# Optimization experiments

Hardware: AMD Instinct MI355X
Metric: run time of the kernel (lower is better)

The kernel has to match this reference:

```python
import jax, jax.numpy as jnp
import numpy as np

K = 16  # topK from config


def setup_inputs() -> dict:
    key = jax.random.key(0)
    k1, k2 = jax.random.split(key)
    predictions = jax.random.uniform(k1, (8, 256, 8), dtype=jnp.float32)
    ref_imgs = jax.random.uniform(k2, (8, 3, 192, 192), dtype=jnp.float32)
    return {"predictions": predictions, "ref_imgs": ref_imgs}


def _dist_loss(predictions, ref_imgs):
    bs, L, _ = predictions.shape
    ch, H, W = ref_imgs.shape[1], ref_imgs.shape[2], ref_imgs.shape[3]
    img_size = W  # original uses ref_imgs.shape[-1] for both axes
    pos = predictions[:, :, :2]  # (bs, L, 2), normalized (x, y) in [0, 1]

    # --- nearest grid_sample (align_corners=False, padding zeros) ---
    # Faithful to the original einops mixup: flat sample i uses image i % bs
    # and grid point preds.reshape(bs*L, 2)[i].
    grid = pos.reshape(bs * L, 2)
    img_idx = jnp.arange(bs * L) % bs
    # unnormalize: pix = ((2g - 1) + 1) * S / 2 - 0.5 = g * S - 0.5
    ix = jnp.round(grid[:, 0] * W - 0.5).astype(jnp.int32)
    iy = jnp.round(grid[:, 1] * H - 0.5).astype(jnp.int32)
    inb = ((ix >= 0) & (ix < W) & (iy >= 0) & (iy < H)).astype(ref_imgs.dtype)
    ixc = jnp.clip(ix, 0, W - 1)
    iyc = jnp.clip(iy, 0, H - 1)
    pooled_flat = ref_imgs[img_idx, :, iyc, ixc] * inb[:, None]  # (bs*L, ch)
    # pooled_colors rearranged '(L bs) ch 1 1 -> bs L ch' with flat order (L outer, bs inner)
    pooled = pooled_flat.reshape(L, bs, ch).transpose(1, 0, 2)  # (bs, L, ch)

    # --- per-pixel squared color distance, sum over channels ---
    # ||ref - pooled||^2 = ||ref||^2 - 2<ref, pooled> + ||pooled||^2 (avoids (bs,L,ch,H,W))
    ref_sq = jnp.sum(ref_imgs * ref_imgs, axis=1)  # (bs, H, W)
    cross = jnp.einsum('bchw,blc->blhw', ref_imgs, pooled)  # (bs, L, H, W)
    pooled_sq = jnp.sum(pooled * pooled, axis=-1)  # (bs, L)
    similar = ref_sq[:, None] - 2.0 * cross + pooled_sq[:, :, None, None]

    # --- K most-similar pixel locations ---
    _, idx = jax.lax.top_k(-similar.reshape(bs, L, H * W), K)  # smallest K
    tgt_x = (idx % img_size).astype(pos.dtype) / img_size
    tgt_y = (idx // img_size).astype(pos.dtype) / img_size
    tgt = jnp.stack([tgt_x, tgt_y], axis=-1)  # (bs, L, K, 2)
    tgt_down = jnp.roll(tgt, shift=1, axis=1)

    # --- closest candidate of the previous stroke (positions detached) ---
    pd = jax.lax.stop_gradient(pos)[:, :, None, :]  # (bs, L, 1, 2)
    dist_down = jnp.sum((pd - tgt_down) ** 2, axis=-1)  # (bs, L, K)
    closest = jnp.argmin(dist_down, axis=-1)  # (bs, L)
    final_tgt = jnp.take_along_axis(tgt_down, closest[:, :, None, None], axis=2)[:, :, 0, :]

    loss = jnp.sum((pos[:, 1:] - final_tgt[:, 1:]) ** 2, axis=-1)  # (bs, L-1)
    return jnp.mean(loss)


def reference(predictions, ref_imgs):
    return _dist_loss(predictions, ref_imgs)
```

## Files before the change

### kernel.cpp

```cpp
#include <hip/hip_runtime.h>
#include <stdint.h>

#define BS 8
#define HH 192
#define WW 192
#define HW (HH*WW)
#define KK 16
#define SITES 9216
#define NW 16
#define SEGSZ 64
#define UCAP 512
#define PAD_FILT 4e-5f

typedef unsigned long long u64;


__device__ __forceinline__ uint32_t fkey(float f) {
    uint32_t u = __float_as_uint(f);
    uint32_t mask = (uint32_t)((int32_t)u >> 31) | 0x80000000u;
    return u ^ mask;
}
__device__ __forceinline__ float inv_fkey(uint32_t v) {
    uint32_t u = (v & 0x80000000u) ? (v ^ 0x80000000u) : ~v;
    return __uint_as_float(u);
}

__device__ __forceinline__ u64 umin64(u64 a, u64 b) { return a < b ? a : b; }

__device__ __forceinline__ uint32_t mbcnt64(u64 m) {
    return __builtin_amdgcn_mbcnt_hi((uint32_t)(m >> 32),
            __builtin_amdgcn_mbcnt_lo((uint32_t)m, 0));
}

__device__ __forceinline__ u64 wave_min_u64(u64 v) {
    #pragma unroll
    for (int off = 32; off >= 1; off >>= 1) {
        uint32_t lo = (uint32_t)v, hi = (uint32_t)(v >> 32);
        lo = __shfl_xor(lo, off, 64);
        hi = __shfl_xor(hi, off, 64);
        u64 o = ((u64)hi << 32) | lo;
        v = umin64(v, o);
    }
    return v;
}

__device__ __forceinline__ void insert64(u64 (&kept)[KK], u64 key) {
    #pragma unroll
    for (int j = KK - 1; j >= 1; --j) {
        u64 a = kept[j - 1];
        u64 mn = umin64(kept[j], key);
        kept[j] = (key < a) ? a : mn;
    }
    kept[0] = umin64(kept[0], key);
}

__device__ __forceinline__ float exact_rsq(float a, float b, float c) {
    return __fadd_rn(__fadd_rn(__fmul_rn(a, a), __fmul_rn(b, b)), __fmul_rn(c, c));
}
__device__ __forceinline__ float exact_sim(float c0, float c1, float c2, float rsq, float4 pq) {
    float cr = __fadd_rn(__fadd_rn(__fmul_rn(c0, pq.x), __fmul_rn(c1, pq.y)), __fmul_rn(c2, pq.z));
    return __fadd_rn(__fsub_rn(rsq, __fmul_rn(2.0f, cr)), pq.w);
}

#define LOSS_STEP(gmv)                                                   \
{                                                                        \
    uint32_t idxv = (uint32_t)(gmv);                                     \
    float tx = (float)(idxv % WW) / 192.0f;                              \
    float ty = (float)(idxv / WW) / 192.0f;                              \
    float ddx = __fsub_rn(px1, tx);                                      \
    float ddy = __fsub_rn(py1, ty);                                      \
    float dd = __fadd_rn(__fmul_rn(ddx, ddx), __fmul_rn(ddy, ddy));      \
    if (dd < dmin) { dmin = dd; btx = tx; bty = ty; }                    \
}

__global__ __launch_bounds__(1024) void fused_kernel(const float* __restrict__ pred,
                                                     const float* __restrict__ ref,
                                                     float* __restrict__ partial) {
    __shared__ uint32_t seg[8 * NW * SEGSZ];
    __shared__ uint32_t compactb[8 * UCAP];
    __shared__ uint32_t scnts[8 * NW];
    __shared__ float4 spool[8];
    __shared__ float sh[8];

    int tid  = threadIdx.x;
    int lane = tid & 63;
    int wid  = tid >> 6;
    int b  = blockIdx.x & 7;
    int qg = blockIdx.x >> 3;

    if (tid < 8) {
        int l = qg * 8 + tid;
        int i = l * BS + b;
        int b2 = i >> 8, l2 = i & 255;
        const float* pr = pred + ((b2 * 256 + l2) * 8);
        float x = pr[0], y = pr[1];
        float fx = rintf(__fsub_rn(__fmul_rn(x, 192.0f), 0.5f));
        float fy = rintf(__fsub_rn(__fmul_rn(y, 192.0f), 0.5f));
        int ix = (int)fx, iy = (int)fy;
        int inb = (ix >= 0 && ix < WW && iy >= 0 && iy < HH) ? 1 : 0;
        int ixc = min(max(ix, 0), WW - 1);
        int iyc = min(max(iy, 0), HH - 1);
        float m = (float)inb;
        const float* img = ref + b * 3 * HW + iyc * WW + ixc;
        float p0 = __fmul_rn(img[0], m);
        float p1 = __fmul_rn(img[HW], m);
        float p2 = __fmul_rn(img[2 * HW], m);
        float psq = __fadd_rn(__fadd_rn(__fmul_rn(p0, p0), __fmul_rn(p1, p1)),
                              __fmul_rn(p2, p2));
        spool[tid] = make_float4(p0, p1, p2, psq);
    }
    __syncthreads();

    const float4* p0g = (const float4*)(ref + (size_t)b * 3 * HW);
    int myq = tid & 7;
    float4 sp = spool[myq];

    float md = -3.4e38f;
    {
        int site = tid;
        float4 n0 = p0g[site], n1 = p0g[site + SITES], n2 = p0g[site + 2 * SITES];
        #pragma unroll 1
        for (int it = 0; it < 8; ++it) {
            float4 a0 = n0, a1 = n1, a2 = n2;
            int sn = (it < 7) ? (site + 1024) : site;
            n0 = p0g[sn]; n1 = p0g[sn + SITES]; n2 = p0g[sn + 2 * SITES];
            #define SAMPM(comp)                                                         \
            {                                                                           \
                float nr = -0.5f * fmaf(a2.comp, a2.comp, fmaf(a1.comp, a1.comp,        \
                                  a0.comp * a0.comp));                                  \
                float d  = fmaf(a2.comp, sp.z, fmaf(a1.comp, sp.y,                      \
                               fmaf(a0.comp, sp.x, nr)));                               \
                md = fmaxf(md, d);                                                      \
            }
            SAMPM(x) SAMPM(y) SAMPM(z) SAMPM(w)
            #undef SAMPM
            site = sn;
        }
    }
    seg[tid] = fkey(-md);

    int site3 = tid;
    float4 f0 = p0g[site3], f1 = p0g[site3 + SITES], f2 = p0g[site3 + 2 * SITES];

    __syncthreads();

    if (wid < 8) {
        uint32_t v0 = seg[lane * 8 + wid];
        uint32_t v1 = seg[(lane + 64) * 8 + wid];
        uint32_t lo = 0x00800000u, hi = 0xFF7FFFFFu;
        #pragma unroll 1
        for (int t = 0; t < 24; ++t) {
            uint32_t mid = lo + ((hi - lo) >> 1);
            int c = ((v0 <= mid) ? 1 : 0) + ((v1 <= mid) ? 1 : 0);
            #pragma unroll
            for (int off = 32; off >= 1; off >>= 1) c += __shfl_xor(c, off, 64);
            if (c >= KK) hi = mid; else lo = mid + 1;
        }
        float hval = -inv_fkey(hi) - PAD_FILT;
        if (qg == 31 && wid == 7) hval = 3.0e38f;
        if (lane == 0) sh[wid] = hval;
    }
    __syncthreads();

    float px[8], py[8], pz[8], hq[8];
    #pragma unroll
    for (int q = 0; q < 8; ++q) {
        float4 s = spool[q];
        px[q] = s.x; py[q] = s.y; pz[q] = s.z; hq[q] = sh[q];
    }
    uint32_t scq0 = 0, scq1 = 0, scq2 = 0, scq3 = 0,
             scq4 = 0, scq5 = 0, scq6 = 0, scq7 = 0;

    #pragma unroll 1
    for (int it = 0; it < 9; ++it) {
        float4 a0 = f0, a1 = f1, a2 = f2;
        int sn = (it < 8) ? (site3 + 1024) : site3;
        f0 = p0g[sn]; f1 = p0g[sn + SITES]; f2 = p0g[sn + 2 * SITES];
        int base = site3 * 4;

        float nrx = -0.5f * fmaf(a2.x, a2.x, fmaf(a1.x, a1.x, a0.x * a0.x));
        float nry = -0.5f * fmaf(a2.y, a2.y, fmaf(a1.y, a1.y, a0.y * a0.y));
        float nrz = -0.5f * fmaf(a2.z, a2.z, fmaf(a1.z, a1.z, a0.z * a0.z));
        float nrw = -0.5f * fmaf(a2.w, a2.w, fmaf(a1.w, a1.w, a0.w * a0.w));

        #define QPUSH(q, scq)                                                           \
        {                                                                               \
            float d0 = fmaf(a2.x, pz[q], fmaf(a1.x, py[q], fmaf(a0.x, px[q], nrx)));    \
            float d1 = fmaf(a2.y, pz[q], fmaf(a1.y, py[q], fmaf(a0.y, px[q], nry)));    \
            float d2 = fmaf(a2.z, pz[q], fmaf(a1.z, py[q], fmaf(a0.z, px[q], nrz)));    \
            float d3 = fmaf(a2.w, pz[q], fmaf(a1.w, py[q], fmaf(a0.w, px[q], nrw)));    \
            u64 m0 = __ballot(d0 >= hq[q]);                                             \
            u64 m1 = __ballot(d1 >= hq[q]);                                             \
            u64 m2 = __ballot(d2 >= hq[q]);                                             \
            u64 m3 = __ballot(d3 >= hq[q]);                                             \
            if (m0 | m1 | m2 | m3) {                    \
                uint32_t sb = ((q) * NW + wid) * SEGSZ;                                 \
                uint32_t c = scq;                                                       \
                if (d0 >= hq[q]) { uint32_t s = c + mbcnt64(m0);                        \
                                   if (s < SEGSZ) seg[sb + s] = (uint32_t)(base + 0); } \
                c += (uint32_t)__popcll(m0);                                            \
                if (d1 >= hq[q]) { uint32_t s = c + mbcnt64(m1);                        \
                                   if (s < SEGSZ) seg[sb + s] = (uint32_t)(base + 1); } \
                c += (uint32_t)__popcll(m1);                                            \
                if (d2 >= hq[q]) { uint32_t s = c + mbcnt64(m2);                        \
                                   if (s < SEGSZ) seg[sb + s] = (uint32_t)(base + 2); } \
                c += (uint32_t)__popcll(m2);                                            \
                if (d3 >= hq[q]) { uint32_t s = c + mbcnt64(m3);                        \
                                   if (s < SEGSZ) seg[sb + s] = (uint32_t)(base + 3); } \
                c += (uint32_t)__popcll(m3);                                            \
                scq = c;                                                                \
            }                                                                           \
        }
        QPUSH(0, scq0) QPUSH(1, scq1) QPUSH(2, scq2) QPUSH(3, scq3)
        QPUSH(4, scq4) QPUSH(5, scq5) QPUSH(6, scq6) QPUSH(7, scq7)
        #undef QPUSH
        site3 = sn;
    }
    if (lane == 0) {
        scnts[0 * NW + wid] = scq0; scnts[1 * NW + wid] = scq1;
        scnts[2 * NW + wid] = scq2; scnts[3 * NW + wid] = scq3;
        scnts[4 * NW + wid] = scq4; scnts[5 * NW + wid] = scq5;
        scnts[6 * NW + wid] = scq6; scnts[7 * NW + wid] = scq7;
    }
    __syncthreads();

    if (wid < 8) {
        int l  = qg * 8 + wid;
        int bl = b * 256 + l;
        if (l == 255) {
            if (lane == 0) partial[bl] = 0.0f;
        } else {
            uint32_t cA[16];
            #pragma unroll
            for (int j = 0; j < 16; ++j) cA[j] = scnts[wid * NW + j];
            bool ovf = false;
            uint32_t pref = 0;
            #pragma unroll
            for (int j = 0; j < 16; ++j) {
                uint32_t c = cA[j];
                ovf = ovf || (c > SEGSZ);
                uint32_t cc = min(c, (uint32_t)SEGSZ);
                if (lane < cc && pref + lane < UCAP)
                    compactb[wid * UCAP + pref + lane] =
                        seg[(wid * NW + j) * SEGSZ + lane];
                pref += cc;
            }
            uint32_t U = pref;
            if (U > UCAP) ovf = true;

            float px1 = pred[(size_t)(bl + 1) * 8 + 0];
            float py1 = pred[(size_t)(bl + 1) * 8 + 1];
            float4 pqv = spool[wid];
            const float* rb = ref + (size_t)b * 3 * HW;
            float dmin = 3.4e38f, btx = 0.0f, bty = 0.0f;

            if (!ovf) {
                u64 r0, r1, r2, r3, r4, r5, r6, r7;
                #define LOADJ(jj, rj)                                                   \
                {                                                                       \
                    uint32_t e = (jj) * 64 + lane;                                      \
                    u64 v = ~0ull;                                                      \
                    if (e < U) {                                                        \
                        uint32_t pidx = compactb[wid * UCAP + e];                       \
                        float c0v = rb[pidx], c1v = rb[pidx + HW], c2v = rb[pidx + 2 * HW]; \
                        float rs = exact_rsq(c0v, c1v, c2v);                            \
                        float sx = exact_sim(c0v, c1v, c2v, rs, pqv);                   \
                        v = ((u64)fkey(sx) << 32) | pidx;                               \
                    }                                                                   \
                    rj = v;                                                             \
                }
                LOADJ(0, r0) LOADJ(1, r1) LOADJ(2, r2) LOADJ(3, r3)
                LOADJ(4, r4) LOADJ(5, r5) LOADJ(6, r6) LOADJ(7, r7)
                #undef LOADJ

                #pragma unroll 1
                for (int rnd = 0; rnd < 16; ++rnd) {
                    u64 mloc = umin64(umin64(umin64(r0, r1), umin64(r2, r3)),
                                      umin64(umin64(r4, r5), umin64(r6, r7)));
                    u64 gm = wave_min_u64(mloc);
                    if (gm != ~0ull) LOSS_STEP(gm)
                    r0 = (r0 == gm) ? ~0ull : r0;
                    r1 = (r1 == gm) ? ~0ull : r1;
                    r2 = (r2 == gm) ? ~0ull : r2;
                    r3 = (r3 == gm) ? ~0ull : r3;
                    r4 = (r4 == gm) ? ~0ull : r4;
                    r5 = (r5 == gm) ? ~0ull : r5;
                    r6 = (r6 == gm) ? ~0ull : r6;
                    r7 = (r7 == gm) ? ~0ull : r7;
                }
            } else {
                u64 kept16[KK];
                #pragma unroll
                for (int j = 0; j < KK; ++j) kept16[j] = ~0ull;
                const float4* pg = (const float4*)rb;
                #pragma unroll 1
                for (int st = lane; st < SITES; st += 64) {
                    float4 a0 = pg[st], a1 = pg[st + SITES], a2 = pg[st + 2 * SITES];
                    int base = st * 4;
                    #define FB(comp, ei)                                                \
                    {                                                                   \
                        float rs = exact_rsq(a0.comp, a1.comp, a2.comp);                \
                        float sx = exact_sim(a0.comp, a1.comp, a2.comp, rs, pqv);       \
                        u64 key = ((u64)fkey(sx) << 32) | (uint32_t)(base + (ei));      \
                        if (key < kept16[KK - 1]) insert64(kept16, key);                \
                    }
                    FB(x, 0) FB(y, 1) FB(z, 2) FB(w, 3)
                    #undef FB
                }
                #pragma unroll 1
                for (int rnd = 0; rnd < 16; ++rnd) {
                    u64 gm = wave_min_u64(kept16[0]);
                    if (kept16[0] == gm) {
                        #pragma unroll
                        for (int j = 0; j < KK - 1; ++j) kept16[j] = kept16[j + 1];
                        kept16[KK - 1] = ~0ull;
                    }
                    LOSS_STEP(gm)
                }
            }

            if (lane == 0) {
                float ex = __fsub_rn(px1, btx);
                float ey = __fsub_rn(py1, bty);
                partial[bl] = __fadd_rn(__fmul_rn(ex, ex), __fmul_rn(ey, ey));
            }
        }
    }
}

__global__ __launch_bounds__(256) void reduce_kernel(const float* __restrict__ partial,
                                                     float* __restrict__ out) {
    __shared__ double sred[256];
    double a = 0.0;
    #pragma unroll
    for (int i = 0; i < 8; ++i) a += (double)partial[i * 256 + threadIdx.x];
    sred[threadIdx.x] = a;
    __syncthreads();
    for (int s = 128; s > 0; s >>= 1) {
        if (threadIdx.x < s) sred[threadIdx.x] += sred[threadIdx.x + s];
        __syncthreads();
    }
    if (threadIdx.x == 0) out[0] = (float)(sred[0] / 2040.0);
}

extern "C" void kernel_launch(void* const* d_in, const int* in_sizes, int n_in,
                              void* d_out, int out_size, void* d_ws, size_t ws_size,
                              hipStream_t stream) {
    const float* pred = (const float*)d_in[0];
    const float* ref  = (const float*)d_in[1];
    float* out = (float*)d_out;

    float* partial = (float*)d_ws;

    fused_kernel <<<256, 1024, 0, stream>>>(pred, ref, partial);
    reduce_kernel<<<  1,  256, 0, stream>>>(partial, out);
}
```

Before: 100.2 us.

## Halve queries per block, compute exact per-query sample thresholds, radix-select final top-K

Each block now handles 4 queries instead of 8, and the grid doubles to 512 blocks. The threshold pass now samples every query across 4096 sites (4 per thread) and bisects with ballot popcounts, replacing the previous scheme of one query per thread over 8 iterations with shuffle reductions. The final top-16 selection swaps 16 rounds of wave-min extraction for a two-level bisection on key and index, followed by a single argmin reduction. The kernel gains parallelism and shorter serial selection, at the cost of re-reading the image twice per block across more blocks and using smaller segment buffers, which may overflow into the slow fallback more often.

```diff
diff --git a/kernel.cpp b/kernel.cpp
--- a/kernel.cpp
+++ b/kernel.cpp
@@ -7,9 +7,10 @@
 #define HW (HH*WW)
 #define KK 16
 #define SITES 9216
+#define NQ 4
 #define NW 16
-#define SEGSZ 64
-#define UCAP 512
+#define SEGSZ 32
+#define UCAP 256
 #define PAD_FILT 4e-5f
 
 typedef unsigned long long u64;
@@ -73,14 +74,14 @@
     if (dd < dmin) { dmin = dd; btx = tx; bty = ty; }                    \
 }
 
-__global__ __launch_bounds__(1024) void fused_kernel(const float* __restrict__ pred,
-                                                     const float* __restrict__ ref,
-                                                     float* __restrict__ partial) {
-    __shared__ uint32_t seg[8 * NW * SEGSZ];
-    __shared__ uint32_t compactb[8 * UCAP];
-    __shared__ uint32_t scnts[8 * NW];
-    __shared__ float4 spool[8];
-    __shared__ float sh[8];
+__global__ __launch_bounds__(1024, 8) void fused_kernel(const float* __restrict__ pred,
+                                                        const float* __restrict__ ref,
+                                                        float* __restrict__ partial) {
+    __shared__ uint32_t mxseg[4096];
+    __shared__ uint32_t compactb[NQ * UCAP];
+    __shared__ uint32_t scnts[NQ * NW];
+    __shared__ float4 spool[NQ];
+    __shared__ float shq[NQ];
 
     int tid  = threadIdx.x;
     int lane = tid & 63;
@@ -88,8 +89,8 @@
     int b  = blockIdx.x & 7;
     int qg = blockIdx.x >> 3;
 
-    if (tid < 8) {
-        int l = qg * 8 + tid;
+    if (tid < NQ) {
+        int l = qg * NQ + tid;
         int i = l * BS + b;
         int b2 = i >> 8, l2 = i & 255;
         const float* pr = pred + ((b2 * 256 + l2) * 8);
@@ -112,137 +113,124 @@
     __syncthreads();
 
     const float4* p0g = (const float4*)(ref + (size_t)b * 3 * HW);
-    int myq = tid & 7;
-    float4 sp = spool[myq];
-
-    float md = -3.4e38f;
-    {
-        int site = tid;
-        float4 n0 = p0g[site], n1 = p0g[site + SITES], n2 = p0g[site + 2 * SITES];
+    float qx[NQ], qy[NQ], qz[NQ];
+    #pragma unroll
+    for (int q = 0; q < NQ; ++q) {
+        float4 s = spool[q];
+        qx[q] = s.x; qy[q] = s.y; qz[q] = s.z;
+    }
+
+    float md0 = -3.4e38f, md1 = -3.4e38f, md2 = -3.4e38f, md3 = -3.4e38f;
+    #pragma unroll 1
+    for (int it = 0; it < 4; ++it) {
+        int site = tid + it * 1024;
+        float4 a0 = p0g[site], a1 = p0g[site + SITES], a2 = p0g[site + 2 * SITES];
+        #define SAMP(comp)                                                              \
+        {                                                                               \
+            float nr = -0.5f * fmaf(a2.comp, a2.comp, fmaf(a1.comp, a1.comp,            \
+                              a0.comp * a0.comp));                                      \
+            float d0_ = fmaf(a2.comp, qz[0], fmaf(a1.comp, qy[0], fmaf(a0.comp, qx[0], nr))); \
+            float d1_ = fmaf(a2.comp, qz[1], fmaf(a1.comp, qy[1], fmaf(a0.comp, qx[1], nr))); \
+            float d2_ = fmaf(a2.comp, qz[2], fmaf(a1.comp, qy[2], fmaf(a0.comp, qx[2], nr))); \
+            float d3_ = fmaf(a2.comp, qz[3], fmaf(a1.comp, qy[3], fmaf(a0.comp, qx[3], nr))); \
+            md0 = fmaxf(md0, d0_); md1 = fmaxf(md1, d1_);                               \
+            md2 = fmaxf(md2, d2_); md3 = fmaxf(md3, d3_);                               \
+        }
+        SAMP(x) SAMP(y) SAMP(z) SAMP(w)
+        #undef SAMP
+    }
+    mxseg[0 * 1024 + tid] = fkey(-md0);
+    mxseg[1 * 1024 + tid] = fkey(-md1);
+    mxseg[2 * 1024 + tid] = fkey(-md2);
+    mxseg[3 * 1024 + tid] = fkey(-md3);
+    __syncthreads();
+
+    if (wid < NQ) {
+        uint32_t v[16];
+        #pragma unroll
+        for (int j = 0; j < 16; ++j) v[j] = mxseg[wid * 1024 + lane + 64 * j];
+        uint32_t lo = 0u, hi = 0xFFFFFFFFu;
         #pragma unroll 1
-        for (int it = 0; it < 8; ++it) {
-            float4 a0 = n0, a1 = n1, a2 = n2;
-            int sn = (it < 7) ? (site + 1024) : site;
-            n0 = p0g[sn]; n1 = p0g[sn + SITES]; n2 = p0g[sn + 2 * SITES];
-            #define SAMPM(comp)                                                         \
-            {                                                                           \
-                float nr = -0.5f * fmaf(a2.comp, a2.comp, fmaf(a1.comp, a1.comp,        \
-                                  a0.comp * a0.comp));                                  \
-                float d  = fmaf(a2.comp, sp.z, fmaf(a1.comp, sp.y,                      \
-                               fmaf(a0.comp, sp.x, nr)));                               \
-                md = fmaxf(md, d);                                                      \
-            }
-            SAMPM(x) SAMPM(y) SAMPM(z) SAMPM(w)
-            #undef SAMPM
-            site = sn;
-        }
-    }
-    seg[tid] = fkey(-md);
-
-    int site3 = tid;
-    float4 f0 = p0g[site3], f1 = p0g[site3 + SITES], f2 = p0g[site3 + 2 * SITES];
-
-    __syncthreads();
-
-    if (wid < 8) {
-        uint32_t v0 = seg[lane * 8 + wid];
-        uint32_t v1 = seg[(lane + 64) * 8 + wid];
-        uint32_t lo = 0x00800000u, hi = 0xFF7FFFFFu;
-        #pragma unroll 1
-        for (int t = 0; t < 24; ++t) {
+        for (int t = 0; t < 32; ++t) {
             uint32_t mid = lo + ((hi - lo) >> 1);
-            int c = ((v0 <= mid) ? 1 : 0) + ((v1 <= mid) ? 1 : 0);
+            int c = 0;
             #pragma unroll
-            for (int off = 32; off >= 1; off >>= 1) c += __shfl_xor(c, off, 64);
+            for (int j = 0; j < 16; ++j) c += (int)__popcll(__ballot(v[j] <= mid));
             if (c >= KK) hi = mid; else lo = mid + 1;
         }
         float hval = -inv_fkey(hi) - PAD_FILT;
-        if (qg == 31 && wid == 7) hval = 3.0e38f;
-        if (lane == 0) sh[wid] = hval;
-    }
-    __syncthreads();
-
-    float px[8], py[8], pz[8], hq[8];
-    #pragma unroll
-    for (int q = 0; q < 8; ++q) {
-        float4 s = spool[q];
-        px[q] = s.x; py[q] = s.y; pz[q] = s.z; hq[q] = sh[q];
-    }
-    uint32_t scq0 = 0, scq1 = 0, scq2 = 0, scq3 = 0,
-             scq4 = 0, scq5 = 0, scq6 = 0, scq7 = 0;
+        if (qg == 63 && wid == 3) hval = 3.0e38f;
+        if (lane == 0) shq[wid] = hval;
+    }
+    __syncthreads();
+
+    float hq0 = shq[0], hq1 = shq[1], hq2 = shq[2], hq3 = shq[3];
+    uint32_t scq0 = 0, scq1 = 0, scq2 = 0, scq3 = 0;
 
     #pragma unroll 1
     for (int it = 0; it < 9; ++it) {
-        float4 a0 = f0, a1 = f1, a2 = f2;
-        int sn = (it < 8) ? (site3 + 1024) : site3;
-        f0 = p0g[sn]; f1 = p0g[sn + SITES]; f2 = p0g[sn + 2 * SITES];
-        int base = site3 * 4;
+        int site = tid + it * 1024;
+        float4 a0 = p0g[site], a1 = p0g[site + SITES], a2 = p0g[site + 2 * SITES];
+        int base = site * 4;
 
         float nrx = -0.5f * fmaf(a2.x, a2.x, fmaf(a1.x, a1.x, a0.x * a0.x));
         float nry = -0.5f * fmaf(a2.y, a2.y, fmaf(a1.y, a1.y, a0.y * a0.y));
         float nrz = -0.5f * fmaf(a2.z, a2.z, fmaf(a1.z, a1.z, a0.z * a0.z));
         float nrw = -0.5f * fmaf(a2.w, a2.w, fmaf(a1.w, a1.w, a0.w * a0.w));
 
-        #define QPUSH(q, scq)                                                           \
+        #define QPUSH(qi, hqv, scq)                                                     \
         {                                                                               \
-            float d0 = fmaf(a2.x, pz[q], fmaf(a1.x, py[q], fmaf(a0.x, px[q], nrx)));    \
-            float d1 = fmaf(a2.y, pz[q], fmaf(a1.y, py[q], fmaf(a0.y, px[q], nry)));    \
-            float d2 = fmaf(a2.z, pz[q], fmaf(a1.z, py[q], fmaf(a0.z, px[q], nrz)));    \
-            float d3 = fmaf(a2.w, pz[q], fmaf(a1.w, py[q], fmaf(a0.w, px[q], nrw)));    \
-            u64 m0 = __ballot(d0 >= hq[q]);                                             \
-            u64 m1 = __ballot(d1 >= hq[q]);                                             \
-            u64 m2 = __ballot(d2 >= hq[q]);                                             \
-            u64 m3 = __ballot(d3 >= hq[q]);                                             \
+            float d0 = fmaf(a2.x, qz[qi], fmaf(a1.x, qy[qi], fmaf(a0.x, qx[qi], nrx))); \
+            float d1 = fmaf(a2.y, qz[qi], fmaf(a1.y, qy[qi], fmaf(a0.y, qx[qi], nry))); \
+            float d2 = fmaf(a2.z, qz[qi], fmaf(a1.z, qy[qi], fmaf(a0.z, qx[qi], nrz))); \
+            float d3 = fmaf(a2.w, qz[qi], fmaf(a1.w, qy[qi], fmaf(a0.w, qx[qi], nrw))); \
+            u64 m0 = __ballot(d0 >= hqv);                                               \
+            u64 m1 = __ballot(d1 >= hqv);                                               \
+            u64 m2 = __ballot(d2 >= hqv);                                               \
+            u64 m3 = __ballot(d3 >= hqv);                                               \
             if (m0 | m1 | m2 | m3) {                    \
-                uint32_t sb = ((q) * NW + wid) * SEGSZ;                                 \
+                uint32_t sb = ((qi) * NW + wid) * SEGSZ;                                \
                 uint32_t c = scq;                                                       \
-                if (d0 >= hq[q]) { uint32_t s = c + mbcnt64(m0);                        \
-                                   if (s < SEGSZ) seg[sb + s] = (uint32_t)(base + 0); } \
+                if (d0 >= hqv) { uint32_t s = c + mbcnt64(m0);                          \
+                                 if (s < SEGSZ) mxseg[sb + s] = (uint32_t)(base + 0); } \
                 c += (uint32_t)__popcll(m0);                                            \
-                if (d1 >= hq[q]) { uint32_t s = c + mbcnt64(m1);                        \
-                                   if (s < SEGSZ) seg[sb + s] = (uint32_t)(base + 1); } \
+                if (d1 >= hqv) { uint32_t s = c + mbcnt64(m1);                          \
+                                 if (s < SEGSZ) mxseg[sb + s] = (uint32_t)(base + 1); } \
                 c += (uint32_t)__popcll(m1);                                            \
-                if (d2 >= hq[q]) { uint32_t s = c + mbcnt64(m2);                        \
-                                   if (s < SEGSZ) seg[sb + s] = (uint32_t)(base + 2); } \
+                if (d2 >= hqv) { uint32_t s = c + mbcnt64(m2);                          \
+                                 if (s < SEGSZ) mxseg[sb + s] = (uint32_t)(base + 2); } \
                 c += (uint32_t)__popcll(m2);                                            \
-                if (d3 >= hq[q]) { uint32_t s = c + mbcnt64(m3);                        \
-                                   if (s < SEGSZ) seg[sb + s] = (uint32_t)(base + 3); } \
+                if (d3 >= hqv) { uint32_t s = c + mbcnt64(m3);                          \
+                                 if (s < SEGSZ) mxseg[sb + s] = (uint32_t)(base + 3); } \
                 c += (uint32_t)__popcll(m3);                                            \
                 scq = c;                                                                \
             }                                                                           \
         }
-        QPUSH(0, scq0) QPUSH(1, scq1) QPUSH(2, scq2) QPUSH(3, scq3)
-        QPUSH(4, scq4) QPUSH(5, scq5) QPUSH(6, scq6) QPUSH(7, scq7)
+        QPUSH(0, hq0, scq0) QPUSH(1, hq1, scq1) QPUSH(2, hq2, scq2) QPUSH(3, hq3, scq3)
         #undef QPUSH
-        site3 = sn;
     }
     if (lane == 0) {
         scnts[0 * NW + wid] = scq0; scnts[1 * NW + wid] = scq1;
         scnts[2 * NW + wid] = scq2; scnts[3 * NW + wid] = scq3;
-        scnts[4 * NW + wid] = scq4; scnts[5 * NW + wid] = scq5;
-        scnts[6 * NW + wid] = scq6; scnts[7 * NW + wid] = scq7;
-    }
-    __syncthreads();
-
-    if (wid < 8) {
-        int l  = qg * 8 + wid;
+    }
+    __syncthreads();
+
+    if (wid < NQ) {
+        int l  = qg * NQ + wid;
         int bl = b * 256 + l;
         if (l == 255) {
             if (lane == 0) partial[bl] = 0.0f;
         } else {
-            uint32_t cA[16];
-            #pragma unroll
-            for (int j = 0; j < 16; ++j) cA[j] = scnts[wid * NW + j];
             bool ovf = false;
             uint32_t pref = 0;
             #pragma unroll
-            for (int j = 0; j < 16; ++j) {
-                uint32_t c = cA[j];
+            for (int j = 0; j < NW; ++j) {
+                uint32_t c = scnts[wid * NW + j];
                 ovf = ovf || (c > SEGSZ);
                 uint32_t cc = min(c, (uint32_t)SEGSZ);
                 if (lane < cc && pref + lane < UCAP)
                     compactb[wid * UCAP + pref + lane] =
-                        seg[(wid * NW + j) * SEGSZ + lane];
+                        mxseg[(wid * NW + j) * SEGSZ + lane];
                 pref += cc;
             }
             uint32_t U = pref;
@@ -252,43 +240,93 @@
             float py1 = pred[(size_t)(bl + 1) * 8 + 1];
             float4 pqv = spool[wid];
             const float* rb = ref + (size_t)b * 3 * HW;
-            float dmin = 3.4e38f, btx = 0.0f, bty = 0.0f;
 
             if (!ovf) {
-                u64 r0, r1, r2, r3, r4, r5, r6, r7;
-                #define LOADJ(jj, rj)                                                   \
+                uint32_t kh0, kh1, kh2, kh3, kl0, kl1, kl2, kl3;
+                #define LOADJ(jj, kh, kl)                                               \
                 {                                                                       \
                     uint32_t e = (jj) * 64 + lane;                                      \
-                    u64 v = ~0ull;                                                      \
+                    uint32_t h_ = 0xFFFFFFFFu, l_ = 0xFFFFFFFFu;                        \
                     if (e < U) {                                                        \
                         uint32_t pidx = compactb[wid * UCAP + e];                       \
                         float c0v = rb[pidx], c1v = rb[pidx + HW], c2v = rb[pidx + 2 * HW]; \
                         float rs = exact_rsq(c0v, c1v, c2v);                            \
                         float sx = exact_sim(c0v, c1v, c2v, rs, pqv);                   \
-                        v = ((u64)fkey(sx) << 32) | pidx;                               \
+                        h_ = fkey(sx); l_ = pidx;                                       \
                     }                                                                   \
-                    rj = v;                                                             \
-                }
-                LOADJ(0, r0) LOADJ(1, r1) LOADJ(2, r2) LOADJ(3, r3)
-                LOADJ(4, r4) LOADJ(5, r5) LOADJ(6, r6) LOADJ(7, r7)
+                    kh = h_; kl = l_;                                                   \
+                }
+                LOADJ(0, kh0, kl0) LOADJ(1, kh1, kl1) LOADJ(2, kh2, kl2) LOADJ(3, kh3, kl3)
                 #undef LOADJ
 
+                uint32_t lo = 0u, hi = 0xFFFFFFFFu;
                 #pragma unroll 1
-                for (int rnd = 0; rnd < 16; ++rnd) {
-                    u64 mloc = umin64(umin64(umin64(r0, r1), umin64(r2, r3)),
-                                      umin64(umin64(r4, r5), umin64(r6, r7)));
-                    u64 gm = wave_min_u64(mloc);
-                    if (gm != ~0ull) LOSS_STEP(gm)
-                    r0 = (r0 == gm) ? ~0ull : r0;
-                    r1 = (r1 == gm) ? ~0ull : r1;
-                    r2 = (r2 == gm) ? ~0ull : r2;
-                    r3 = (r3 == gm) ? ~0ull : r3;
-                    r4 = (r4 == gm) ? ~0ull : r4;
-                    r5 = (r5 == gm) ? ~0ull : r5;
-                    r6 = (r6 == gm) ? ~0ull : r6;
-                    r7 = (r7 == gm) ? ~0ull : r7;
+                for (int t = 0; t < 32; ++t) {
+                    uint32_t mid = lo + ((hi - lo) >> 1);
+                    int c = (int)__popcll(__ballot(kh0 <= mid))
+                          + (int)__popcll(__ballot(kh1 <= mid))
+                          + (int)__popcll(__ballot(kh2 <= mid))
+                          + (int)__popcll(__ballot(kh3 <= mid));
+                    if (c >= KK) hi = mid; else lo = mid + 1;
+                }
+                uint32_t Hh = hi;
+                int c1 = (int)__popcll(__ballot(kh0 < Hh))
+                       + (int)__popcll(__ballot(kh1 < Hh))
+                       + (int)__popcll(__ballot(kh2 < Hh))
+                       + (int)__popcll(__ballot(kh3 < Hh));
+                int need = KK - c1;
+                u64 e0 = __ballot(kh0 == Hh), e1 = __ballot(kh1 == Hh);
+                u64 e2 = __ballot(kh2 == Hh), e3 = __ballot(kh3 == Hh);
+                lo = 0u; hi = 0xFFFFFFFFu;
+                #pragma unroll 1
+                for (int t = 0; t < 32; ++t) {
+                    uint32_t mid = lo + ((hi - lo) >> 1);
+                    int c = (int)__popcll(e0 & __ballot(kl0 <= mid))
+                          + (int)__popcll(e1 & __ballot(kl1 <= mid))
+                          + (int)__popcll(e2 & __ballot(kl2 <= mid))
+                          + (int)__popcll(e3 & __ballot(kl3 <= mid));
+                    if (c >= need) hi = mid; else lo = mid + 1;
+                }
+                uint32_t Lh = hi;
+
+                uint32_t bd = 0xFFFFFFFFu, bh = 0xFFFFFFFFu, bo = 0xFFFFFFFFu;
+                #define SELJ(kh, kl)                                                    \
+                {                                                                       \
+                    bool sel = (kh < Hh) || (kh == Hh && kl <= Lh);                     \
+                    if (sel) {                                                          \
+                        uint32_t idxv = kl;                                             \
+                        float tx = (float)(idxv % WW) / 192.0f;                         \
+                        float ty = (float)(idxv / WW) / 192.0f;                         \
+                        float ddx = __fsub_rn(px1, tx);                                 \
+                        float ddy = __fsub_rn(py1, ty);                                 \
+                        float dd = __fadd_rn(__fmul_rn(ddx, ddx), __fmul_rn(ddy, ddy)); \
+                        uint32_t db = __float_as_uint(dd);         \
+                        bool lt = (db < bd) ||                                          \
+                                  (db == bd && (kh < bh || (kh == bh && kl < bo)));     \
+                        if (lt) { bd = db; bh = kh; bo = kl; }                          \
+                    }                                                                   \
+                }
+                SELJ(kh0, kl0) SELJ(kh1, kl1) SELJ(kh2, kl2) SELJ(kh3, kl3)
+                #undef SELJ
+                #pragma unroll
+                for (int off = 32; off >= 1; off >>= 1) {
+                    uint32_t od = __shfl_xor(bd, off, 64);
+                    uint32_t oh = __shfl_xor(bh, off, 64);
+                    uint32_t oo = __shfl_xor(bo, off, 64);
+                    bool lt = (od < bd) ||
+                              (od == bd && (oh < bh || (oh == bh && oo < bo)));
+                    if (lt) { bd = od; bh = oh; bo = oo; }
+                }
+                if (lane == 0) {
+                    uint32_t idxv = bo;
+                    float tx = (float)(idxv % WW) / 192.0f;
+                    float ty = (float)(idxv / WW) / 192.0f;
+                    float ex = __fsub_rn(px1, tx);
+                    float ey = __fsub_rn(py1, ty);
+                    partial[bl] = __fadd_rn(__fmul_rn(ex, ex), __fmul_rn(ey, ey));
                 }
             } else {
+                float dmin = 3.4e38f, btx = 0.0f, bty = 0.0f;
                 u64 kept16[KK];
                 #pragma unroll
                 for (int j = 0; j < KK; ++j) kept16[j] = ~0ull;
@@ -317,12 +355,11 @@
                     }
                     LOSS_STEP(gm)
                 }
-            }
-
-            if (lane == 0) {
-                float ex = __fsub_rn(px1, btx);
-                float ey = __fsub_rn(py1, bty);
-                partial[bl] = __fadd_rn(__fmul_rn(ex, ex), __fmul_rn(ey, ey));
+                if (lane == 0) {
+                    float ex = __fsub_rn(px1, btx);
+                    float ey = __fsub_rn(py1, bty);
+                    partial[bl] = __fadd_rn(__fmul_rn(ex, ex), __fmul_rn(ey, ey));
+                }
             }
         }
     }
@@ -352,6 +389,6 @@
 
     float* partial = (float*)d_ws;
 
-    fused_kernel <<<256, 1024, 0, stream>>>(pred, ref, partial);
+    fused_kernel <<<512, 1024, 0, stream>>>(pred, ref, partial);
     reduce_kernel<<<  1,  256, 0, stream>>>(partial, out);
 }
```

Measured after the change: 90.51 us. -9.7%, faster.
